# Performance work log

Measured on AMD Instinct MI355X. Metric: run time of the kernel, lower is better.

The kernel has to match this reference:

```python
import jax, jax.numpy as jnp
import numpy as np

B, N, M = 512, 1024, 128
OUT_DIM, MOLVEC_DIM, IN_DIM = 256, 256, 512


def setup_inputs() -> dict:
    key = jax.random.key(0)
    ks = jax.random.split(key, 6)
    X = jax.random.normal(ks[0], (B, N, OUT_DIM), dtype=jnp.float32)
    molvec = jax.random.normal(ks[1], (B, MOLVEC_DIM), dtype=jnp.float32)
    idx_M = jax.random.randint(ks[2], (B, M), 0, N, dtype=jnp.int64)
    # Xavier-normal-ish scaled linear weights (torch layout: [out_features, in_features])
    fan_in1 = MOLVEC_DIM + OUT_DIM
    W1 = jax.random.normal(ks[3], (IN_DIM, fan_in1), dtype=jnp.float32) * jnp.sqrt(2.0 / (fan_in1 + IN_DIM))
    b1 = jnp.zeros((IN_DIM,), dtype=jnp.float32)
    W2 = jax.random.normal(ks[4], (IN_DIM, IN_DIM), dtype=jnp.float32) * jnp.sqrt(2.0 / (IN_DIM + IN_DIM))
    b2 = jnp.zeros((IN_DIM,), dtype=jnp.float32)
    return {"X": X, "molvec": molvec, "idx_M": idx_M, "W1": W1, "b1": b1, "W2": W2, "b2": b2}


def reference(X, molvec, idx_M, W1, b1, W2, b2):
    # Batched gather: replaces the per-sample index_select loop. [B, M, OUT_DIM]
    target_x = jnp.take_along_axis(X, idx_M[:, :, None], axis=1)
    # Broadcast molvec to each masked position and concat. [B, M, OUT_DIM+MOLVEC_DIM]
    mv = jnp.broadcast_to(molvec[:, None, :], (X.shape[0], idx_M.shape[1], molvec.shape[-1]))
    concat_x = jnp.concatenate([target_x, mv], axis=-1)
    # 2-layer MLP (fc1 -> relu -> fc2)
    h = jax.nn.relu(jnp.einsum('bmd,id->bmi', concat_x, W1) + b1)
    pred = jnp.einsum('bmi,oi->bmo', h, W2) + b2
    return pred.reshape(X.shape[0] * idx_M.shape[1], -1)
```

## Files before the change

kernel.cpp:

```cpp
#include <hip/hip_runtime.h>
#include <hip/hip_bf16.h>

#define BB 512
#define NN 1024
#define MM 128
#define OUTD 256
#define MOLD 256
#define IND 512
#define K1 512
#define RROWS 65536

typedef float f32x4 __attribute__((ext_vector_type(4)));
typedef short s16x8 __attribute__((ext_vector_type(8)));
typedef __bf16 bf16x8 __attribute__((ext_vector_type(8)));

#define AS_GLOBAL const __attribute__((address_space(1))) void
#define AS_LDS __attribute__((address_space(3))) void

__device__ __forceinline__ unsigned short f2bf(float f) {
    unsigned int u = __builtin_bit_cast(unsigned int, f);
    u = (u + 0x7fffu + ((u >> 16) & 1u)) >> 16;
    return (unsigned short)u;
}

__global__ __launch_bounds__(256) void prep_weights(
    const float* __restrict__ W1, const float* __restrict__ W2,
    unsigned short* __restrict__ W1b, unsigned short* __restrict__ W2b) {
    int i = blockIdx.x * 256 + threadIdx.x;
    float4 a = ((const float4*)W1)[i];
    ushort4 pa;
    pa.x = f2bf(a.x); pa.y = f2bf(a.y); pa.z = f2bf(a.z); pa.w = f2bf(a.w);
    ((ushort4*)W1b)[i] = pa;
    float4 b = ((const float4*)W2)[i];
    ushort4 pb;
    pb.x = f2bf(b.x); pb.y = f2bf(b.y); pb.z = f2bf(b.z); pb.w = f2bf(b.w);
    ((ushort4*)W2b)[i] = pb;
}

__global__ __launch_bounds__(256) void gemm1_kernel(
    const float* __restrict__ X, const float* __restrict__ mol,
    const int* __restrict__ idxp, const unsigned short* __restrict__ W1b,
    const float* __restrict__ b1, unsigned short* __restrict__ H) {
    __shared__ __align__(16) unsigned short Asm[128 * 32];
    __shared__ __align__(16) unsigned short Bsm[128 * 32];

    const int t = threadIdx.x;
    const int lane = t & 63, w = t >> 6;
    const int b = blockIdx.x;
    const int n0 = blockIdx.y * 128;
    const int wr = (w >> 1) * 64, wc = (w & 1) * 64;
    const int lr = lane & 15, quad = lane >> 4;

    const int arow = t >> 1;
    const int acol = (t & 1) * 16;
    const int idx = idxp[b * MM + arow];
    const float* Xrow = X + ((size_t)b * NN + idx) * OUTD;
    const float* mvrow = mol + (size_t)b * MOLD;

    f32x4 acc[4][4];
#pragma unroll
    for (int mi = 0; mi < 4; ++mi)
#pragma unroll
        for (int ni = 0; ni < 4; ++ni) acc[mi][ni] = {0.f, 0.f, 0.f, 0.f};

    for (int ki = 0; ki < 16; ++ki) {
        const int kt = ki * 32;
        const float* src = (kt < OUTD) ? (Xrow + kt + acol) : (mvrow + (kt - OUTD) + acol);
        const float4* s4 = (const float4*)src;
        float4 v0 = s4[0], v1 = s4[1], v2 = s4[2], v3 = s4[3];
        unsigned short* dst = &Asm[arow * 32 + acol];
        ushort4 p;
        p.x = f2bf(v0.x); p.y = f2bf(v0.y); p.z = f2bf(v0.z); p.w = f2bf(v0.w);
        *(ushort4*)(dst + 0) = p;
        p.x = f2bf(v1.x); p.y = f2bf(v1.y); p.z = f2bf(v1.z); p.w = f2bf(v1.w);
        *(ushort4*)(dst + 4) = p;
        p.x = f2bf(v2.x); p.y = f2bf(v2.y); p.z = f2bf(v2.z); p.w = f2bf(v2.w);
        *(ushort4*)(dst + 8) = p;
        p.x = f2bf(v3.x); p.y = f2bf(v3.y); p.z = f2bf(v3.z); p.w = f2bf(v3.w);
        *(ushort4*)(dst + 12) = p;
#pragma unroll
        for (int j = 0; j < 2; ++j) {
            const int cidx = j * 4 + w;
            const int s = cidx * 64 + lane;
            const unsigned short* gb = W1b + (size_t)(n0 + (s >> 2)) * K1 + kt + (s & 3) * 8;
            __builtin_amdgcn_global_load_lds((AS_GLOBAL*)gb, (AS_LDS*)(Bsm + cidx * 512), 16, 0, 0);
        }
        __syncthreads();
        s16x8 af[4], bfr[4];
#pragma unroll
        for (int i = 0; i < 4; ++i)
            af[i] = *(const s16x8*)&Asm[(wr + i * 16 + lr) * 32 + quad * 8];
#pragma unroll
        for (int i = 0; i < 4; ++i)
            bfr[i] = *(const s16x8*)&Bsm[(wc + i * 16 + lr) * 32 + quad * 8];
#pragma unroll
        for (int mi = 0; mi < 4; ++mi)
#pragma unroll
            for (int ni = 0; ni < 4; ++ni)
                acc[mi][ni] = __builtin_amdgcn_mfma_f32_16x16x32_bf16(
                    __builtin_bit_cast(bf16x8, af[mi]),
                    __builtin_bit_cast(bf16x8, bfr[ni]), acc[mi][ni], 0, 0, 0);
        __syncthreads();
    }

    float bias[4];
#pragma unroll
    for (int ni = 0; ni < 4; ++ni) bias[ni] = b1[n0 + wc + ni * 16 + lr];
    const int row0 = b * 128;
#pragma unroll
    for (int mi = 0; mi < 4; ++mi) {
#pragma unroll
        for (int ni = 0; ni < 4; ++ni) {
            const int gcol = n0 + wc + ni * 16 + lr;
#pragma unroll
            for (int rr = 0; rr < 4; ++rr) {
                const int grow = row0 + wr + mi * 16 + quad * 4 + rr;
                float v = acc[mi][ni][rr] + bias[ni];
                v = v > 0.f ? v : 0.f;
                H[(size_t)grow * IND + gcol] = f2bf(v);
            }
        }
    }
}

__global__ __launch_bounds__(256) void gemm2_kernel(
    const unsigned short* __restrict__ Hb, const unsigned short* __restrict__ W2b,
    const float* __restrict__ b2, float* __restrict__ out) {
    __shared__ __align__(16) unsigned short Asm[128 * 32];
    __shared__ __align__(16) unsigned short Bsm[128 * 32];

    const int t = threadIdx.x;
    const int lane = t & 63, w = t >> 6;
    const int row0 = blockIdx.x * 128;
    const int n0 = blockIdx.y * 128;
    const int wr = (w >> 1) * 64, wc = (w & 1) * 64;
    const int lr = lane & 15, quad = lane >> 4;

    f32x4 acc[4][4];
#pragma unroll
    for (int mi = 0; mi < 4; ++mi)
#pragma unroll
        for (int ni = 0; ni < 4; ++ni) acc[mi][ni] = {0.f, 0.f, 0.f, 0.f};

    for (int ki = 0; ki < 16; ++ki) {
        const int kt = ki * 32;
#pragma unroll
        for (int j = 0; j < 2; ++j) {
            const int cidx = j * 4 + w;
            const int s = cidx * 64 + lane;
            const unsigned short* ga = Hb + (size_t)(row0 + (s >> 2)) * IND + kt + (s & 3) * 8;
            __builtin_amdgcn_global_load_lds((AS_GLOBAL*)ga, (AS_LDS*)(Asm + cidx * 512), 16, 0, 0);
            const unsigned short* gb = W2b + (size_t)(n0 + (s >> 2)) * IND + kt + (s & 3) * 8;
            __builtin_amdgcn_global_load_lds((AS_GLOBAL*)gb, (AS_LDS*)(Bsm + cidx * 512), 16, 0, 0);
        }
        __syncthreads();
        s16x8 af[4], bfr[4];
#pragma unroll
        for (int i = 0; i < 4; ++i)
            af[i] = *(const s16x8*)&Asm[(wr + i * 16 + lr) * 32 + quad * 8];
#pragma unroll
        for (int i = 0; i < 4; ++i)
            bfr[i] = *(const s16x8*)&Bsm[(wc + i * 16 + lr) * 32 + quad * 8];
#pragma unroll
        for (int mi = 0; mi < 4; ++mi)
#pragma unroll
            for (int ni = 0; ni < 4; ++ni)
                acc[mi][ni] = __builtin_amdgcn_mfma_f32_16x16x32_bf16(
                    __builtin_bit_cast(bf16x8, af[mi]),
                    __builtin_bit_cast(bf16x8, bfr[ni]), acc[mi][ni], 0, 0, 0);
        __syncthreads();
    }

    float bias[4];
#pragma unroll
    for (int ni = 0; ni < 4; ++ni) bias[ni] = b2[n0 + wc + ni * 16 + lr];
#pragma unroll
    for (int mi = 0; mi < 4; ++mi) {
#pragma unroll
        for (int ni = 0; ni < 4; ++ni) {
            const int gcol = n0 + wc + ni * 16 + lr;
#pragma unroll
            for (int rr = 0; rr < 4; ++rr) {
                const int grow = row0 + wr + mi * 16 + quad * 4 + rr;
                out[(size_t)grow * IND + gcol] = acc[mi][ni][rr] + bias[ni];
            }
        }
    }
}

extern "C" void kernel_launch(void* const* d_in, const int* in_sizes, int n_in,
                              void* d_out, int out_size, void* d_ws, size_t ws_size,
                              hipStream_t stream) {
    const float* X = (const float*)d_in[0];
    const float* mol = (const float*)d_in[1];
    const int* idx = (const int*)d_in[2];
    const float* W1 = (const float*)d_in[3];
    const float* b1 = (const float*)d_in[4];
    const float* W2 = (const float*)d_in[5];
    const float* b2 = (const float*)d_in[6];
    float* out = (float*)d_out;

    unsigned short* W1b = (unsigned short*)d_ws;
    unsigned short* W2b = W1b + 512 * 512;
    unsigned short* H = W2b + 512 * 512;

    prep_weights<<<256, 256, 0, stream>>>(W1, W2, W1b, W2b);
    gemm1_kernel<<<dim3(BB, IND / 128), 256, 0, stream>>>(X, mol, idx, W1b, b1, H);
    gemm2_kernel<<<dim3(RROWS / 128, IND / 128), 256, 0, stream>>>(H, W2b, b2, out);
}
```

Before: 730.3 us.

## Split gather into separate bf16 staging kernel, use BK=64 with XOR-swizzled LDS tiles

Moves the gather/concat/bf16 conversion out of gemm1 into a dedicated kernel that writes a bf16 A matrix to workspace. Both GEMMs can then load A and B with direct global-to-LDS loads. The K tile grows from 32 to 64, which halves the barrier count, and the LDS rows are XOR-swizzled to avoid bank conflicts on fragment reads. The cost is an extra kernel launch plus a 64 MB bf16 intermediate write and read, and it removes the per-k-step conversion work from gemm1.

```diff
diff --git a/kernel.cpp b/kernel.cpp
--- a/kernel.cpp
+++ b/kernel.cpp
@@ -9,6 +9,8 @@
 #define IND 512
 #define K1 512
 #define RROWS 65536
+#define BK 64
+#define SROW 64
 
 typedef float f32x4 __attribute__((ext_vector_type(4)));
 typedef short s16x8 __attribute__((ext_vector_type(8)));
@@ -37,97 +39,32 @@
     ((ushort4*)W2b)[i] = pb;
 }
 
+__global__ __launch_bounds__(256) void gather_kernel(
+    const float* __restrict__ X, const float* __restrict__ mol,
+    const int* __restrict__ idxp, unsigned short* __restrict__ Abuf) {
+    const int t = threadIdx.x;
+    const int lane = t & 63;
+    const int row = blockIdx.x * 4 + (t >> 6);
+    const int b = row >> 7, m = row & 127;
+    const int idx = idxp[b * MM + m];
+    const float4* xr = (const float4*)(X + ((size_t)b * NN + idx) * OUTD);
+    const float4* mv = (const float4*)(mol + (size_t)b * MOLD);
+    unsigned short* dst = Abuf + (size_t)row * K1;
+    float4 v = xr[lane];
+    ushort4 p;
+    p.x = f2bf(v.x); p.y = f2bf(v.y); p.z = f2bf(v.z); p.w = f2bf(v.w);
+    ((ushort4*)dst)[lane] = p;
+    v = mv[lane];
+    p.x = f2bf(v.x); p.y = f2bf(v.y); p.z = f2bf(v.z); p.w = f2bf(v.w);
+    ((ushort4*)(dst + OUTD))[lane] = p;
+}
+
+
 __global__ __launch_bounds__(256) void gemm1_kernel(
-    const float* __restrict__ X, const float* __restrict__ mol,
-    const int* __restrict__ idxp, const unsigned short* __restrict__ W1b,
+    const unsigned short* __restrict__ Ab, const unsigned short* __restrict__ W1b,
     const float* __restrict__ b1, unsigned short* __restrict__ H) {
-    __shared__ __align__(16) unsigned short Asm[128 * 32];
-    __shared__ __align__(16) unsigned short Bsm[128 * 32];
-
-    const int t = threadIdx.x;
-    const int lane = t & 63, w = t >> 6;
-    const int b = blockIdx.x;
-    const int n0 = blockIdx.y * 128;
-    const int wr = (w >> 1) * 64, wc = (w & 1) * 64;
-    const int lr = lane & 15, quad = lane >> 4;
-
-    const int arow = t >> 1;
-    const int acol = (t & 1) * 16;
-    const int idx = idxp[b * MM + arow];
-    const float* Xrow = X + ((size_t)b * NN + idx) * OUTD;
-    const float* mvrow = mol + (size_t)b * MOLD;
-
-    f32x4 acc[4][4];
-#pragma unroll
-    for (int mi = 0; mi < 4; ++mi)
-#pragma unroll
-        for (int ni = 0; ni < 4; ++ni) acc[mi][ni] = {0.f, 0.f, 0.f, 0.f};
-
-    for (int ki = 0; ki < 16; ++ki) {
-        const int kt = ki * 32;
-        const float* src = (kt < OUTD) ? (Xrow + kt + acol) : (mvrow + (kt - OUTD) + acol);
-        const float4* s4 = (const float4*)src;
-        float4 v0 = s4[0], v1 = s4[1], v2 = s4[2], v3 = s4[3];
-        unsigned short* dst = &Asm[arow * 32 + acol];
-        ushort4 p;
-        p.x = f2bf(v0.x); p.y = f2bf(v0.y); p.z = f2bf(v0.z); p.w = f2bf(v0.w);
-        *(ushort4*)(dst + 0) = p;
-        p.x = f2bf(v1.x); p.y = f2bf(v1.y); p.z = f2bf(v1.z); p.w = f2bf(v1.w);
-        *(ushort4*)(dst + 4) = p;
-        p.x = f2bf(v2.x); p.y = f2bf(v2.y); p.z = f2bf(v2.z); p.w = f2bf(v2.w);
-        *(ushort4*)(dst + 8) = p;
-        p.x = f2bf(v3.x); p.y = f2bf(v3.y); p.z = f2bf(v3.z); p.w = f2bf(v3.w);
-        *(ushort4*)(dst + 12) = p;
-#pragma unroll
-        for (int j = 0; j < 2; ++j) {
-            const int cidx = j * 4 + w;
-            const int s = cidx * 64 + lane;
-            const unsigned short* gb = W1b + (size_t)(n0 + (s >> 2)) * K1 + kt + (s & 3) * 8;
-            __builtin_amdgcn_global_load_lds((AS_GLOBAL*)gb, (AS_LDS*)(Bsm + cidx * 512), 16, 0, 0);
-        }
-        __syncthreads();
-        s16x8 af[4], bfr[4];
-#pragma unroll
-        for (int i = 0; i < 4; ++i)
-            af[i] = *(const s16x8*)&Asm[(wr + i * 16 + lr) * 32 + quad * 8];
-#pragma unroll
-        for (int i = 0; i < 4; ++i)
-            bfr[i] = *(const s16x8*)&Bsm[(wc + i * 16 + lr) * 32 + quad * 8];
-#pragma unroll
-        for (int mi = 0; mi < 4; ++mi)
-#pragma unroll
-            for (int ni = 0; ni < 4; ++ni)
-                acc[mi][ni] = __builtin_amdgcn_mfma_f32_16x16x32_bf16(
-                    __builtin_bit_cast(bf16x8, af[mi]),
-                    __builtin_bit_cast(bf16x8, bfr[ni]), acc[mi][ni], 0, 0, 0);
-        __syncthreads();
-    }
-
-    float bias[4];
-#pragma unroll
-    for (int ni = 0; ni < 4; ++ni) bias[ni] = b1[n0 + wc + ni * 16 + lr];
-    const int row0 = b * 128;
-#pragma unroll
-    for (int mi = 0; mi < 4; ++mi) {
-#pragma unroll
-        for (int ni = 0; ni < 4; ++ni) {
-            const int gcol = n0 + wc + ni * 16 + lr;
-#pragma unroll
-            for (int rr = 0; rr < 4; ++rr) {
-                const int grow = row0 + wr + mi * 16 + quad * 4 + rr;
-                float v = acc[mi][ni][rr] + bias[ni];
-                v = v > 0.f ? v : 0.f;
-                H[(size_t)grow * IND + gcol] = f2bf(v);
-            }
-        }
-    }
-}
-
-__global__ __launch_bounds__(256) void gemm2_kernel(
-    const unsigned short* __restrict__ Hb, const unsigned short* __restrict__ W2b,
-    const float* __restrict__ b2, float* __restrict__ out) {
-    __shared__ __align__(16) unsigned short Asm[128 * 32];
-    __shared__ __align__(16) unsigned short Bsm[128 * 32];
+    __shared__ __align__(16) unsigned short Asm[128 * SROW];
+    __shared__ __align__(16) unsigned short Bsm[128 * SROW];
 
     const int t = threadIdx.x;
     const int lane = t & 63, w = t >> 6;
@@ -135,6 +72,8 @@
     const int n0 = blockIdx.y * 128;
     const int wr = (w >> 1) * 64, wc = (w & 1) * 64;
     const int lr = lane & 15, quad = lane >> 4;
+    const int srow = lane >> 3;
+    const int sseg = (lane & 7) ^ srow;
 
     f32x4 acc[4][4];
 #pragma unroll
@@ -142,32 +81,107 @@
 #pragma unroll
         for (int ni = 0; ni < 4; ++ni) acc[mi][ni] = {0.f, 0.f, 0.f, 0.f};
 
-    for (int ki = 0; ki < 16; ++ki) {
-        const int kt = ki * 32;
-#pragma unroll
-        for (int j = 0; j < 2; ++j) {
-            const int cidx = j * 4 + w;
-            const int s = cidx * 64 + lane;
-            const unsigned short* ga = Hb + (size_t)(row0 + (s >> 2)) * IND + kt + (s & 3) * 8;
-            __builtin_amdgcn_global_load_lds((AS_GLOBAL*)ga, (AS_LDS*)(Asm + cidx * 512), 16, 0, 0);
-            const unsigned short* gb = W2b + (size_t)(n0 + (s >> 2)) * IND + kt + (s & 3) * 8;
-            __builtin_amdgcn_global_load_lds((AS_GLOBAL*)gb, (AS_LDS*)(Bsm + cidx * 512), 16, 0, 0);
-        }
-        __syncthreads();
-        s16x8 af[4], bfr[4];
-#pragma unroll
-        for (int i = 0; i < 4; ++i)
-            af[i] = *(const s16x8*)&Asm[(wr + i * 16 + lr) * 32 + quad * 8];
-#pragma unroll
-        for (int i = 0; i < 4; ++i)
-            bfr[i] = *(const s16x8*)&Bsm[(wc + i * 16 + lr) * 32 + quad * 8];
-#pragma unroll
-        for (int mi = 0; mi < 4; ++mi)
-#pragma unroll
-            for (int ni = 0; ni < 4; ++ni)
-                acc[mi][ni] = __builtin_amdgcn_mfma_f32_16x16x32_bf16(
-                    __builtin_bit_cast(bf16x8, af[mi]),
-                    __builtin_bit_cast(bf16x8, bfr[ni]), acc[mi][ni], 0, 0, 0);
+    for (int ki = 0; ki < K1 / BK; ++ki) {
+        const int kt = ki * BK;
+#pragma unroll
+        for (int j = 0; j < 4; ++j) {
+            const int c = j * 4 + w;
+            const unsigned short* ga = Ab + (size_t)(row0 + c * 8 + srow) * K1 + kt + sseg * 8;
+            __builtin_amdgcn_global_load_lds((AS_GLOBAL*)ga, (AS_LDS*)(Asm + c * 512), 16, 0, 0);
+            const unsigned short* gb = W1b + (size_t)(n0 + c * 8 + srow) * K1 + kt + sseg * 8;
+            __builtin_amdgcn_global_load_lds((AS_GLOBAL*)gb, (AS_LDS*)(Bsm + c * 512), 16, 0, 0);
+        }
+        __syncthreads();
+#pragma unroll
+        for (int h = 0; h < 2; ++h) {
+            s16x8 af[4], bfr[4];
+#pragma unroll
+            for (int i = 0; i < 4; ++i) {
+                const int ra = wr + i * 16 + lr;
+                af[i] = *(const s16x8*)&Asm[ra * SROW + (((h * 4 + quad) ^ (lr & 7)) * 8)];
+                const int rb = wc + i * 16 + lr;
+                bfr[i] = *(const s16x8*)&Bsm[rb * SROW + (((h * 4 + quad) ^ (lr & 7)) * 8)];
+            }
+#pragma unroll
+            for (int mi = 0; mi < 4; ++mi)
+#pragma unroll
+                for (int ni = 0; ni < 4; ++ni)
+                    acc[mi][ni] = __builtin_amdgcn_mfma_f32_16x16x32_bf16(
+                        __builtin_bit_cast(bf16x8, af[mi]),
+                        __builtin_bit_cast(bf16x8, bfr[ni]), acc[mi][ni], 0, 0, 0);
+        }
+        __syncthreads();
+    }
+
+    float bias[4];
+#pragma unroll
+    for (int ni = 0; ni < 4; ++ni) bias[ni] = b1[n0 + wc + ni * 16 + lr];
+#pragma unroll
+    for (int mi = 0; mi < 4; ++mi) {
+#pragma unroll
+        for (int ni = 0; ni < 4; ++ni) {
+            const int gcol = n0 + wc + ni * 16 + lr;
+#pragma unroll
+            for (int rr = 0; rr < 4; ++rr) {
+                const int grow = row0 + wr + mi * 16 + quad * 4 + rr;
+                float v = acc[mi][ni][rr] + bias[ni];
+                v = v > 0.f ? v : 0.f;
+                H[(size_t)grow * IND + gcol] = f2bf(v);
+            }
+        }
+    }
+}
+
+__global__ __launch_bounds__(256) void gemm2_kernel(
+    const unsigned short* __restrict__ Hb, const unsigned short* __restrict__ W2b,
+    const float* __restrict__ b2, float* __restrict__ out) {
+    __shared__ __align__(16) unsigned short Asm[128 * SROW];
+    __shared__ __align__(16) unsigned short Bsm[128 * SROW];
+
+    const int t = threadIdx.x;
+    const int lane = t & 63, w = t >> 6;
+    const int row0 = blockIdx.x * 128;
+    const int n0 = blockIdx.y * 128;
+    const int wr = (w >> 1) * 64, wc = (w & 1) * 64;
+    const int lr = lane & 15, quad = lane >> 4;
+    const int srow = lane >> 3;
+    const int sseg = (lane & 7) ^ srow;
+
+    f32x4 acc[4][4];
+#pragma unroll
+    for (int mi = 0; mi < 4; ++mi)
+#pragma unroll
+        for (int ni = 0; ni < 4; ++ni) acc[mi][ni] = {0.f, 0.f, 0.f, 0.f};
+
+    for (int ki = 0; ki < IND / BK; ++ki) {
+        const int kt = ki * BK;
+#pragma unroll
+        for (int j = 0; j < 4; ++j) {
+            const int c = j * 4 + w;
+            const unsigned short* ga = Hb + (size_t)(row0 + c * 8 + srow) * IND + kt + sseg * 8;
+            __builtin_amdgcn_global_load_lds((AS_GLOBAL*)ga, (AS_LDS*)(Asm + c * 512), 16, 0, 0);
+            const unsigned short* gb = W2b + (size_t)(n0 + c * 8 + srow) * IND + kt + sseg * 8;
+            __builtin_amdgcn_global_load_lds((AS_GLOBAL*)gb, (AS_LDS*)(Bsm + c * 512), 16, 0, 0);
+        }
+        __syncthreads();
+#pragma unroll
+        for (int h = 0; h < 2; ++h) {
+            s16x8 af[4], bfr[4];
+#pragma unroll
+            for (int i = 0; i < 4; ++i) {
+                const int ra = wr + i * 16 + lr;
+                af[i] = *(const s16x8*)&Asm[ra * SROW + (((h * 4 + quad) ^ (lr & 7)) * 8)];
+                const int rb = wc + i * 16 + lr;
+                bfr[i] = *(const s16x8*)&Bsm[rb * SROW + (((h * 4 + quad) ^ (lr & 7)) * 8)];
+            }
+#pragma unroll
+            for (int mi = 0; mi < 4; ++mi)
+#pragma unroll
+                for (int ni = 0; ni < 4; ++ni)
+                    acc[mi][ni] = __builtin_amdgcn_mfma_f32_16x16x32_bf16(
+                        __builtin_bit_cast(bf16x8, af[mi]),
+                        __builtin_bit_cast(bf16x8, bfr[ni]), acc[mi][ni], 0, 0, 0);
+        }
         __syncthreads();
     }
 
@@ -202,9 +216,11 @@
 
     unsigned short* W1b = (unsigned short*)d_ws;
     unsigned short* W2b = W1b + 512 * 512;
-    unsigned short* H = W2b + 512 * 512;
+    unsigned short* Abuf = W2b + 512 * 512;
+    unsigned short* H = Abuf + (size_t)RROWS * K1;
 
     prep_weights<<<256, 256, 0, stream>>>(W1, W2, W1b, W2b);
-    gemm1_kernel<<<dim3(BB, IND / 128), 256, 0, stream>>>(X, mol, idx, W1b, b1, H);
+    gather_kernel<<<RROWS / 4, 256, 0, stream>>>(X, mol, idx, Abuf);
+    gemm1_kernel<<<dim3(RROWS / 128, IND / 128), 256, 0, stream>>>(Abuf, W1b, b1, H);
     gemm2_kernel<<<dim3(RROWS / 128, IND / 128), 256, 0, stream>>>(H, W2b, b2, out);
 }
```

Result: slower. 746.1 us (+2.2%).
